# Kernel optimization log

Measured on AMD Instinct MI355X. Metric: run time of the kernel, lower is better.

Reference implementation:

```python
import jax, jax.numpy as jnp
import numpy as np

N_NODES = 50000
N_EDGES = 800000
DIM = 256
HEADS = 8
DIM_OUT = 32  # per-head; dim_inner = HEADS*DIM_OUT = 256


def setup_inputs() -> dict:
    key = jax.random.key(0)
    ks = jax.random.split(key, 9)
    s = 1.0 / np.sqrt(DIM)
    inner = HEADS * DIM_OUT
    return {
        "x": jax.random.normal(ks[0], (N_NODES, DIM), dtype=jnp.float32),
        "Wq": jax.random.uniform(ks[1], (DIM, inner), jnp.float32, -s, s),
        "bq": jax.random.uniform(ks[2], (inner,), jnp.float32, -s, s),
        "Wk": jax.random.uniform(ks[3], (DIM, inner), jnp.float32, -s, s),
        "bk": jax.random.uniform(ks[4], (inner,), jnp.float32, -s, s),
        "Wv": jax.random.uniform(ks[5], (DIM, inner), jnp.float32, -s, s),
        "bv": jax.random.uniform(ks[6], (inner,), jnp.float32, -s, s),
        "src": jax.random.randint(ks[7], (N_EDGES,), 0, N_NODES),
        "dst": jax.random.randint(ks[8], (N_EDGES,), 0, N_NODES),
    }


def reference(x, Wq, bq, Wk, bk, Wv, bv, src, dst):
    n = x.shape[0]
    q = (x @ Wq + bq).reshape(n, HEADS, DIM_OUT)
    k = (x @ Wk + bk).reshape(n, HEADS, DIM_OUT)
    v = (x @ Wv + bv).reshape(n, HEADS, DIM_OUT)
    # edge-wise u_dot_v: dot of src query with dst key, per head -> [E, H]
    scores = jnp.einsum('ehd,ehd->eh', q[src], k[dst]) / jnp.sqrt(
        jnp.asarray(DIM_OUT, dtype=x.dtype))
    # segment softmax over incoming edges of each destination node
    m = jax.ops.segment_max(scores, dst, num_segments=n)  # [N, H]
    m = jnp.where(jnp.isfinite(m), m, 0.0)
    e = jnp.exp(scores - m[dst])
    z = jax.ops.segment_sum(e, dst, num_segments=n)  # [N, H]
    p = e / jnp.maximum(z[dst], 1e-16)  # [E, H]
    # u_mul_e_sum: sum over incoming edges of src values weighted by attn
    out = jax.ops.segment_sum(v[src] * p[:, :, None], dst, num_segments=n)
    return out.reshape(n, HEADS * DIM_OUT)  # concat=True
```

## Files before the change

### kernel.cpp

```cpp
#include <hip/hip_runtime.h>
#include <math.h>

#define N_NODES 50000
#define N_EDGES 800000
#define DIM 256
#define HEADS 8
#define DIM_OUT 32
#define INNER 256
#define M_PAD 50048

typedef __attribute__((ext_vector_type(8))) short bf16x8;
typedef __attribute__((ext_vector_type(4))) float f32x4;
typedef __attribute__((ext_vector_type(2))) float f32x2;

__device__ __forceinline__ unsigned short f2bf(float f) {
    unsigned u = __float_as_uint(f);
    unsigned r = (u + 0x7FFFu + ((u >> 16) & 1u)) >> 16;
    return (unsigned short)r;
}

__device__ __forceinline__ f32x2 up2(unsigned u) {
    f32x2 r;
    r.x = __uint_as_float(u << 16);
    r.y = __uint_as_float(u & 0xFFFF0000u);
    return r;
}
__device__ __forceinline__ void up2x4(uint4 r, f32x2* o) {
    o[0] = up2(r.x); o[1] = up2(r.y); o[2] = up2(r.z); o[3] = up2(r.w);
}

__device__ __forceinline__ void gll16(const void* g, void* l) {
    __builtin_amdgcn_global_load_lds(
        (const __attribute__((address_space(1))) unsigned*)(uintptr_t)g,
        (__attribute__((address_space(3))) unsigned*)(unsigned)(uintptr_t)l,
        16, 0, 0);
}

#define NB_CONVX 6256
#define NB_CONVW 768
#define NB_HIST  3125
__global__ __launch_bounds__(256) void prep(
    const float* __restrict__ x,
    const float* __restrict__ Wq, const float* __restrict__ Wk,
    const float* __restrict__ Wv,
    const int* __restrict__ dst,
    unsigned short* __restrict__ xbf, unsigned short* __restrict__ Wt,
    int* __restrict__ deg)
{
    int b = blockIdx.x;
    if (b < NB_CONVX) {
        size_t i8 = ((size_t)b * 256 + threadIdx.x) * 8;
        unsigned short h[8];
        if (i8 < (size_t)N_NODES * 256) {
            float4 a = *(const float4*)(x + i8);
            float4 c = *(const float4*)(x + i8 + 4);
            h[0]=f2bf(a.x); h[1]=f2bf(a.y); h[2]=f2bf(a.z); h[3]=f2bf(a.w);
            h[4]=f2bf(c.x); h[5]=f2bf(c.y); h[6]=f2bf(c.z); h[7]=f2bf(c.w);
        } else {
            #pragma unroll
            for (int j = 0; j < 8; j++) h[j] = 0;
        }
        uint4 o;
        o.x = (unsigned)h[0] | ((unsigned)h[1] << 16);
        o.y = (unsigned)h[2] | ((unsigned)h[3] << 16);
        o.z = (unsigned)h[4] | ((unsigned)h[5] << 16);
        o.w = (unsigned)h[6] | ((unsigned)h[7] << 16);
        *(uint4*)(xbf + i8) = o;
    } else if (b < NB_CONVX + NB_CONVW) {
        int idx = (b - NB_CONVX) * 256 + threadIdx.x;
        int z = idx >> 16, r = idx & 65535;
        int k = r >> 8, n = r & 255;
        const float* W = (z == 0) ? Wq : (z == 1) ? Wk : Wv;
        Wt[(size_t)z * 65536 + n * 256 + k] = f2bf(W[k * 256 + n]);
    } else {
        int e = (b - NB_CONVX - NB_CONVW) * 256 + threadIdx.x;
        if (e < N_EDGES) atomicAdd(deg + dst[e], 1);
    }
}

#define GEMM_NWG 1173
__global__ __launch_bounds__(512) void gemm_qkv(
    const unsigned short* __restrict__ xbf,
    const unsigned short* __restrict__ Wt,
    const float* __restrict__ bq, const float* __restrict__ bk,
    const float* __restrict__ bv,
    unsigned short* __restrict__ q, unsigned short* __restrict__ k,
    unsigned short* __restrict__ v)
{
    int hw = blockIdx.x;
    int xcd = hw & 7, pos = hw >> 3;
    int lid = (xcd < 5 ? xcd * 147 : 5 * 147 + (xcd - 5) * 146) + pos;
    int panel = lid / 3;
    int z = lid - panel * 3;
    const int row0 = panel * 128;

    const int t = threadIdx.x;
    const unsigned short* Wz = Wt + (size_t)z * 65536;
    const float* bias = (z == 0) ? bq : (z == 1) ? bk : bv;
    unsigned short* C = (z == 0) ? q : (z == 1) ? k : v;

    __shared__ __align__(16) short As[128 * 32];
    __shared__ __align__(16) short Bs[256 * 32];

    const int wave = t >> 6;
    const int lane = t & 63;
    const int wm = (wave & 1) * 64;
    const int wn = (wave >> 1) * 64;
    const int lr = lane & 15;
    const int lg = lane >> 4;
    const int srow = lane >> 2;
    const int sch  = lane & 3;

    f32x4 acc[4][4] = {};

    for (int k0 = 0; k0 < 256; k0 += 32) {
        gll16(xbf + (size_t)(row0 + wave * 16 + srow) * 256 + k0 + sch * 8,
              As + wave * 512);
        #pragma unroll
        for (int c = 0; c < 2; c++) {
            gll16(Wz + (size_t)(wave * 32 + c * 16 + srow) * 256 + k0 + sch * 8,
                  Bs + wave * 1024 + c * 512);
        }
        __syncthreads();

        bf16x8 af[4], bfr[4];
        #pragma unroll
        for (int mi = 0; mi < 4; mi++)
            af[mi] = *(const bf16x8*)&As[(wm + mi * 16 + lr) * 32 + lg * 8];
        #pragma unroll
        for (int ni = 0; ni < 4; ni++)
            bfr[ni] = *(const bf16x8*)&Bs[(wn + ni * 16 + lr) * 32 + lg * 8];
        #pragma unroll
        for (int mi = 0; mi < 4; mi++)
            #pragma unroll
            for (int ni = 0; ni < 4; ni++)
                acc[mi][ni] = __builtin_amdgcn_mfma_f32_16x16x32_bf16(
                    af[mi], bfr[ni], acc[mi][ni], 0, 0, 0);
        __syncthreads();
    }

    #pragma unroll
    for (int mi = 0; mi < 4; mi++) {
        #pragma unroll
        for (int ni = 0; ni < 4; ni++) {
            int gcol = wn + ni * 16 + lr;
            float bb = bias[gcol];
            #pragma unroll
            for (int r = 0; r < 4; r++) {
                int grow = row0 + wm + mi * 16 + lg * 4 + r;
                if (grow < N_NODES)
                    C[(size_t)grow * 256 + gcol] = f2bf(acc[mi][ni][r] + bb);
            }
        }
    }
}

__global__ __launch_bounds__(1024) void scan_deg(
    const int* __restrict__ deg, int* __restrict__ rowptr)
{
    __shared__ int wsum[16];
    __shared__ int wpre[16];
    int t = threadIdx.x;
    int wid = t >> 6, ln = t & 63;
    int carry = 0;
    for (int base = 0; base < N_NODES; base += 4096) {
        int i4 = base + t * 4;
        int4 dv = {0, 0, 0, 0};
        if (i4 < N_NODES) dv = *(const int4*)(deg + i4);
        int sum = dv.x + dv.y + dv.z + dv.w;
        int inc = sum;
        #pragma unroll
        for (int off = 1; off < 64; off <<= 1) {
            int u = __shfl_up(inc, off);
            if (ln >= off) inc += u;
        }
        if (ln == 63) wsum[wid] = inc;
        __syncthreads();
        if (wid == 0 && ln < 16) {
            int s = wsum[ln];
            int p = s;
            #pragma unroll
            for (int off = 1; off < 16; off <<= 1) {
                int u = __shfl_up(p, off);
                if (ln >= off) p += u;
            }
            wpre[ln] = p - s;
        }
        __syncthreads();
        if (i4 < N_NODES) {
            int r = carry + wpre[wid] + (inc - sum);
            r += dv.x; rowptr[i4 + 1] = r;
            r += dv.y; rowptr[i4 + 2] = r;
            r += dv.z; rowptr[i4 + 3] = r;
            r += dv.w; rowptr[i4 + 4] = r;
        }
        carry += wpre[15] + wsum[15];
        __syncthreads();
    }
    if (t == 0) rowptr[0] = 0;
}

__global__ __launch_bounds__(256) void csr_scatter(
    const int* __restrict__ src, const int* __restrict__ dst,
    const int* __restrict__ rowptr,
    int* __restrict__ deg, int* __restrict__ edge_src)
{
    int e = blockIdx.x * 256 + threadIdx.x;
    if (e >= N_EDGES) return;
    int d = dst[e];
    int old = atomicSub(deg + d, 1);
    edge_src[rowptr[d] + old - 1] = src[e];
}

__global__ __launch_bounds__(256) void node_attn(
    const unsigned short* __restrict__ qbf,
    const unsigned short* __restrict__ kbf,
    const unsigned short* __restrict__ vbf,
    const int* __restrict__ rowptr, const int* __restrict__ edge_src,
    float* __restrict__ out)
{
    int node = blockIdx.x * 4 + (threadIdx.x >> 6);
    int lane = threadIdx.x & 63;
    if (node >= N_NODES) return;
    const int half = lane >> 5;
    const int l = lane & 31;

    int beg = rowptr[node], end = rowptr[node + 1];
    int deg = end - beg;

    float* op = out + (size_t)node * 256 + l * 8;
    if (deg <= 0) {
        if (half == 0) {
            float4 z4 = {0.f, 0.f, 0.f, 0.f};
            *(float4*)op = z4;
            *(float4*)(op + 4) = z4;
        }
        return;
    }

    f32x2 kf2[4];
    up2x4(*(const uint4*)(kbf + (size_t)node * 256 + l * 8), kf2);

    const unsigned short* qrow = qbf + l * 8;
    const unsigned short* vrow = vbf + l * 8;

    const float SC = 0.17677669529663687f * 1.4426950408889634f;

    int U = (deg + 1) >> 1;
    U = ((U + 2) / 3) * 3;
    U = __builtin_amdgcn_readfirstlane(U);

    const int i0 = beg + half;
    const int last = end - 1;

    int tmp0 = edge_src[min(i0,     last)];
    int tmp1 = edge_src[min(i0 + 2, last)];
    int idC  = edge_src[min(i0 + 4, last)];
    int idA  = edge_src[min(i0 + 6, last)];
    int idB  = 0;
    uint4 qA = *(const uint4*)(qrow + (size_t)tmp0 * 256);
    uint4 vA = *(const uint4*)(vrow + (size_t)tmp0 * 256);
    uint4 qB = *(const uint4*)(qrow + (size_t)tmp1 * 256);
    uint4 vB = *(const uint4*)(vrow + (size_t)tmp1 * 256);
    uint4 qC, vC;

    float m = -1e30f, zsum = 0.0f;
    f32x2 af2[4] = {};

#define BODY(QW, VW, QL, VL, IDL, IDF, P)                                    \
    do {                                                                     \
        size_t off_ = (size_t)(IDL) * 256;                                   \
        QL = *(const uint4*)(qrow + off_);                                   \
        VL = *(const uint4*)(vrow + off_);                                   \
        int vi_ = i0 + 2 * t + 2 * (P);                                      \
        IDF = edge_src[min(vi_ + 8, last)];                                  \
        f32x2 qf_[4], vf_[4];                                                \
        up2x4(QW, qf_);                                                      \
        up2x4(VW, vf_);                                                      \
        f32x2 d_ = qf_[0] * kf2[0];                                          \
        d_ += qf_[1] * kf2[1];                                               \
        d_ += qf_[2] * kf2[2];                                               \
        d_ += qf_[3] * kf2[3];                                               \
        float s_ = d_.x + d_.y;                                              \
        s_ += __shfl_xor(s_, 1);                                             \
        s_ += __shfl_xor(s_, 2);                                             \
        bool ok_ = vi_ < end;                                                \
        float sc_ = ok_ ? s_ * SC : -1e30f;                                  \
        float mn_ = fmaxf(m, sc_);                                           \
        float w_ = exp2f(sc_ - mn_);                                         \
        w_ = ok_ ? w_ : 0.0f;                                                \
        float al_ = exp2f(m - mn_);                                          \
        zsum = zsum * al_ + w_;                                              \
        f32x2 a2_ = {al_, al_}, w2_ = {w_, w_};                              \
        af2[0] = af2[0] * a2_ + vf_[0] * w2_;                                \
        af2[1] = af2[1] * a2_ + vf_[1] * w2_;                                \
        af2[2] = af2[2] * a2_ + vf_[2] * w2_;                                \
        af2[3] = af2[3] * a2_ + vf_[3] * w2_;                                \
        m = mn_;                                                             \
    } while (0)

    for (int t = 0; t < U; t += 3) {
        BODY(qA, vA, qC, vC, idC, idB, 0);
        BODY(qB, vB, qA, vA, idA, idC, 1);
        BODY(qC, vC, qB, vB, idB, idA, 2);
    }
#undef BODY

    float mo = __shfl_xor(m, 32);
    float mt = fmaxf(m, mo);
    float scale = exp2f(m - mt);
    zsum *= scale;
    zsum += __shfl_xor(zsum, 32);
    #pragma unroll
    for (int j = 0; j < 4; j++) {
        af2[j].x = af2[j].x * scale;
        af2[j].y = af2[j].y * scale;
        af2[j].x += __shfl_xor(af2[j].x, 32);
        af2[j].y += __shfl_xor(af2[j].y, 32);
    }

    float inv = 1.0f / fmaxf(zsum, 1e-16f);
    if (half == 0) {
        float4 o0 = {af2[0].x * inv, af2[0].y * inv, af2[1].x * inv, af2[1].y * inv};
        float4 o1 = {af2[2].x * inv, af2[2].y * inv, af2[3].x * inv, af2[3].y * inv};
        *(float4*)op = o0;
        *(float4*)(op + 4) = o1;
    }
}

extern "C" void kernel_launch(void* const* d_in, const int* in_sizes, int n_in,
                              void* d_out, int out_size, void* d_ws, size_t ws_size,
                              hipStream_t stream) {
    const float* x  = (const float*)d_in[0];
    const float* Wq = (const float*)d_in[1];
    const float* bq = (const float*)d_in[2];
    const float* Wk = (const float*)d_in[3];
    const float* bk = (const float*)d_in[4];
    const float* Wv = (const float*)d_in[5];
    const float* bv = (const float*)d_in[6];
    const int* src  = (const int*)d_in[7];
    const int* dst  = (const int*)d_in[8];
    float* out = (float*)d_out;

    unsigned short* qbf = (unsigned short*)d_ws;
    unsigned short* kbf = qbf + (size_t)N_NODES * INNER;
    unsigned short* vbf = kbf + (size_t)N_NODES * INNER;
    unsigned short* xbf = vbf + (size_t)N_NODES * INNER;
    unsigned short* Wt  = xbf + (size_t)M_PAD * INNER;
    int* deg      = (int*)(Wt + 3 * 65536);
    int* rowptr   = deg + N_NODES;
    int* edge_src = rowptr + (N_NODES + 1);

    hipMemsetAsync(deg, 0, (size_t)N_NODES * sizeof(int), stream);

    prep<<<NB_CONVX + NB_CONVW + NB_HIST, 256, 0, stream>>>(
        x, Wq, Wk, Wv, dst, xbf, Wt, deg);

    gemm_qkv<<<GEMM_NWG, 512, 0, stream>>>(xbf, Wt, bq, bk, bv, qbf, kbf, vbf);

    scan_deg<<<1, 1024, 0, stream>>>(deg, rowptr);
    csr_scatter<<<(N_EDGES + 255) / 256, 256, 0, stream>>>(
        src, dst, rowptr, deg, edge_src);

    node_attn<<<(N_NODES + 3) / 4, 256, 0, stream>>>(
        qbf, kbf, vbf, rowptr, edge_src, out);
}
```

Baseline: 360.0 us.

## Fuse degree scan into GEMM launch, record edge ranks, double-buffer GEMM LDS

The degree prefix scan moves into block 0 of the QKV GEMM launch, removing a separate single-block kernel launch and letting it overlap with the GEMM. The histogram atomics now save each edge's slot rank, so the CSR scatter no longer needs a second atomic pass over the degrees. The GEMM K loop is double-buffered in LDS so the next tile's global-to-LDS loads can overlap the current MFMA work, at the cost of twice the shared memory per workgroup. The new rank array adds 800K ints of extra writes and reads.

```diff
diff --git a/kernel.cpp b/kernel.cpp
--- a/kernel.cpp
+++ b/kernel.cpp
@@ -45,7 +45,7 @@
     const float* __restrict__ Wv,
     const int* __restrict__ dst,
     unsigned short* __restrict__ xbf, unsigned short* __restrict__ Wt,
-    int* __restrict__ deg)
+    int* __restrict__ deg, int* __restrict__ rank)
 {
     int b = blockIdx.x;
     if (b < NB_CONVX) {
@@ -74,7 +74,7 @@
         Wt[(size_t)z * 65536 + n * 256 + k] = f2bf(W[k * 256 + n]);
     } else {
         int e = (b - NB_CONVX - NB_CONVW) * 256 + threadIdx.x;
-        if (e < N_EDGES) atomicAdd(deg + dst[e], 1);
+        if (e < N_EDGES) rank[e] = atomicAdd(deg + dst[e], 1);
     }
 }
 
@@ -85,22 +85,63 @@
     const float* __restrict__ bq, const float* __restrict__ bk,
     const float* __restrict__ bv,
     unsigned short* __restrict__ q, unsigned short* __restrict__ k,
-    unsigned short* __restrict__ v)
+    unsigned short* __restrict__ v,
+    const int* __restrict__ deg, int* __restrict__ rowptr)
 {
-    int hw = blockIdx.x;
+    const int t = threadIdx.x;
+
+    if (blockIdx.x == 0) {
+        __shared__ int wsum[8];
+        __shared__ int wpre[9];
+        int wid = t >> 6, ln = t & 63;
+        int carry = 0;
+        for (int base = 0; base < N_NODES; base += 2048) {
+            int i4 = base + t * 4;
+            int4 dv = {0, 0, 0, 0};
+            if (i4 < N_NODES) dv = *(const int4*)(deg + i4);
+            int sum = dv.x + dv.y + dv.z + dv.w;
+            int inc = sum;
+            #pragma unroll
+            for (int off = 1; off < 64; off <<= 1) {
+                int u = __shfl_up(inc, off);
+                if (ln >= off) inc += u;
+            }
+            if (ln == 63) wsum[wid] = inc;
+            __syncthreads();
+            if (t == 0) {
+                int a = 0;
+                #pragma unroll
+                for (int j = 0; j < 8; j++) { wpre[j] = a; a += wsum[j]; }
+                wpre[8] = a;
+            }
+            __syncthreads();
+            if (i4 < N_NODES) {
+                int r = carry + wpre[wid] + (inc - sum);
+                r += dv.x; rowptr[i4 + 1] = r;
+                r += dv.y; rowptr[i4 + 2] = r;
+                r += dv.z; rowptr[i4 + 3] = r;
+                r += dv.w; rowptr[i4 + 4] = r;
+            }
+            carry += wpre[8];
+            __syncthreads();
+        }
+        if (t == 0) rowptr[0] = 0;
+        return;
+    }
+
+    int hw = blockIdx.x - 1;
     int xcd = hw & 7, pos = hw >> 3;
     int lid = (xcd < 5 ? xcd * 147 : 5 * 147 + (xcd - 5) * 146) + pos;
     int panel = lid / 3;
     int z = lid - panel * 3;
     const int row0 = panel * 128;
 
-    const int t = threadIdx.x;
     const unsigned short* Wz = Wt + (size_t)z * 65536;
     const float* bias = (z == 0) ? bq : (z == 1) ? bk : bv;
     unsigned short* C = (z == 0) ? q : (z == 1) ? k : v;
 
-    __shared__ __align__(16) short As[128 * 32];
-    __shared__ __align__(16) short Bs[256 * 32];
+    __shared__ __align__(16) short As[2][128 * 32];
+    __shared__ __align__(16) short Bs[2][256 * 32];
 
     const int wave = t >> 6;
     const int lane = t & 63;
@@ -113,31 +154,37 @@
 
     f32x4 acc[4][4] = {};
 
-    for (int k0 = 0; k0 < 256; k0 += 32) {
-        gll16(xbf + (size_t)(row0 + wave * 16 + srow) * 256 + k0 + sch * 8,
-              As + wave * 512);
-        #pragma unroll
-        for (int c = 0; c < 2; c++) {
-            gll16(Wz + (size_t)(wave * 32 + c * 16 + srow) * 256 + k0 + sch * 8,
-                  Bs + wave * 1024 + c * 512);
-        }
+#define STAGE(B, K)                                                          \
+    do {                                                                     \
+        gll16(xbf + (size_t)(row0 + wave * 16 + srow) * 256 + (K) + sch * 8, \
+              &As[B][wave * 512]);                                           \
+        gll16(Wz + (size_t)(wave * 32 + srow) * 256 + (K) + sch * 8,         \
+              &Bs[B][wave * 1024]);                                          \
+        gll16(Wz + (size_t)(wave * 32 + 16 + srow) * 256 + (K) + sch * 8,    \
+              &Bs[B][wave * 1024 + 512]);                                    \
+    } while (0)
+
+    STAGE(0, 0);
+    #pragma unroll
+    for (int s = 0; s < 8; s++) {
+        const int cur = s & 1;
         __syncthreads();
-
+        if (s < 7) STAGE(cur ^ 1, (s + 1) * 32);
         bf16x8 af[4], bfr[4];
         #pragma unroll
         for (int mi = 0; mi < 4; mi++)
-            af[mi] = *(const bf16x8*)&As[(wm + mi * 16 + lr) * 32 + lg * 8];
+            af[mi] = *(const bf16x8*)&As[cur][(wm + mi * 16 + lr) * 32 + lg * 8];
         #pragma unroll
         for (int ni = 0; ni < 4; ni++)
-            bfr[ni] = *(const bf16x8*)&Bs[(wn + ni * 16 + lr) * 32 + lg * 8];
+            bfr[ni] = *(const bf16x8*)&Bs[cur][(wn + ni * 16 + lr) * 32 + lg * 8];
         #pragma unroll
         for (int mi = 0; mi < 4; mi++)
             #pragma unroll
             for (int ni = 0; ni < 4; ni++)
                 acc[mi][ni] = __builtin_amdgcn_mfma_f32_16x16x32_bf16(
                     af[mi], bfr[ni], acc[mi][ni], 0, 0, 0);
-        __syncthreads();
-    }
+    }
+#undef STAGE
 
     #pragma unroll
     for (int mi = 0; mi < 4; mi++) {
@@ -155,61 +202,14 @@
     }
 }
 
-__global__ __launch_bounds__(1024) void scan_deg(
-    const int* __restrict__ deg, int* __restrict__ rowptr)
-{
-    __shared__ int wsum[16];
-    __shared__ int wpre[16];
-    int t = threadIdx.x;
-    int wid = t >> 6, ln = t & 63;
-    int carry = 0;
-    for (int base = 0; base < N_NODES; base += 4096) {
-        int i4 = base + t * 4;
-        int4 dv = {0, 0, 0, 0};
-        if (i4 < N_NODES) dv = *(const int4*)(deg + i4);
-        int sum = dv.x + dv.y + dv.z + dv.w;
-        int inc = sum;
-        #pragma unroll
-        for (int off = 1; off < 64; off <<= 1) {
-            int u = __shfl_up(inc, off);
-            if (ln >= off) inc += u;
-        }
-        if (ln == 63) wsum[wid] = inc;
-        __syncthreads();
-        if (wid == 0 && ln < 16) {
-            int s = wsum[ln];
-            int p = s;
-            #pragma unroll
-            for (int off = 1; off < 16; off <<= 1) {
-                int u = __shfl_up(p, off);
-                if (ln >= off) p += u;
-            }
-            wpre[ln] = p - s;
-        }
-        __syncthreads();
-        if (i4 < N_NODES) {
-            int r = carry + wpre[wid] + (inc - sum);
-            r += dv.x; rowptr[i4 + 1] = r;
-            r += dv.y; rowptr[i4 + 2] = r;
-            r += dv.z; rowptr[i4 + 3] = r;
-            r += dv.w; rowptr[i4 + 4] = r;
-        }
-        carry += wpre[15] + wsum[15];
-        __syncthreads();
-    }
-    if (t == 0) rowptr[0] = 0;
-}
-
 __global__ __launch_bounds__(256) void csr_scatter(
     const int* __restrict__ src, const int* __restrict__ dst,
-    const int* __restrict__ rowptr,
-    int* __restrict__ deg, int* __restrict__ edge_src)
+    const int* __restrict__ rowptr, const int* __restrict__ rank,
+    int* __restrict__ edge_src)
 {
     int e = blockIdx.x * 256 + threadIdx.x;
     if (e >= N_EDGES) return;
-    int d = dst[e];
-    int old = atomicSub(deg + d, 1);
-    edge_src[rowptr[d] + old - 1] = src[e];
+    edge_src[rowptr[dst[e]] + rank[e]] = src[e];
 }
 
 __global__ __launch_bounds__(256) void node_attn(
@@ -350,17 +350,18 @@
     int* deg      = (int*)(Wt + 3 * 65536);
     int* rowptr   = deg + N_NODES;
     int* edge_src = rowptr + (N_NODES + 1);
+    int* rank     = edge_src + N_EDGES;
 
     hipMemsetAsync(deg, 0, (size_t)N_NODES * sizeof(int), stream);
 
     prep<<<NB_CONVX + NB_CONVW + NB_HIST, 256, 0, stream>>>(
-        x, Wq, Wk, Wv, dst, xbf, Wt, deg);
-
-    gemm_qkv<<<GEMM_NWG, 512, 0, stream>>>(xbf, Wt, bq, bk, bv, qbf, kbf, vbf);
-
-    scan_deg<<<1, 1024, 0, stream>>>(deg, rowptr);
+        x, Wq, Wk, Wv, dst, xbf, Wt, deg, rank);
+
+    gemm_qkv<<<GEMM_NWG + 1, 512, 0, stream>>>(
+        xbf, Wt, bq, bk, bv, qbf, kbf, vbf, deg, rowptr);
+
     csr_scatter<<<(N_EDGES + 255) / 256, 256, 0, stream>>>(
-        src, dst, rowptr, deg, edge_src);
+        src, dst, rowptr, rank, edge_src);
 
     node_attn<<<(N_NODES + 3) / 4, 256, 0, stream>>>(
         qbf, kbf, vbf, rowptr, edge_src, out);
```

New measurement: 325.4 us. 9.6% less time.
